# Kernel tuning notes

Measured on AMD Instinct MI355X. Metric: run time of the kernel, lower is better.

Reference implementation:

```python
import jax, jax.numpy as jnp
import numpy as np

N, D, H, E, K = 16384, 1024, 4096, 8, 2
EPS = 1e-5


def setup_inputs() -> dict:
    key = jax.random.key(0)
    ks = jax.random.split(key, 12)
    s = 0.02
    return {
        "x": jax.random.normal(ks[0], (N, D), dtype=jnp.float32),
        "ln_g": jnp.ones((D,), jnp.float32),
        "ln_b": jnp.zeros((D,), jnp.float32),
        "r_w1": jax.random.normal(ks[1], (D, H // 2), jnp.float32) * s,
        "r_b1": jnp.zeros((H // 2,), jnp.float32),
        "r_w2": jax.random.normal(ks[2], (H // 2, E), jnp.float32) * s,
        "r_b2": jnp.zeros((E,), jnp.float32),
        "e_w1": jax.random.normal(ks[3], (E, D, H), jnp.float32) * s,
        "e_b1": jnp.zeros((E, H), jnp.float32),
        "e_w2": jax.random.normal(ks[4], (E, H, D), jnp.float32) * s,
        "e_b2": jnp.zeros((E, D), jnp.float32),
    }


def reference(x, ln_g, ln_b, r_w1, r_b1, r_w2, r_b2, e_w1, e_b1, e_w2, e_b2):
    # LayerNorm
    mu = jnp.mean(x, axis=-1, keepdims=True)
    var = jnp.mean(jnp.square(x - mu), axis=-1, keepdims=True)
    xn = (x - mu) * jax.lax.rsqrt(var + EPS) * ln_g + ln_b  # [N, D]

    # Router: Linear -> ReLU -> Linear -> softmax -> top-k, renormalize
    logits = jax.nn.relu(xn @ r_w1 + r_b1) @ r_w2 + r_b2  # [N, E]
    probs = jax.nn.softmax(logits, axis=-1)
    vals, idx = jax.lax.top_k(probs, K)  # [N, K]
    vals = vals / jnp.sum(vals, axis=-1, keepdims=True)

    # Dense expert dispatch: loop over fixed small E, weight by combine gate
    out = jnp.zeros_like(x)
    for e in range(E):
        gate = jnp.sum(vals * (idx == e).astype(vals.dtype), axis=-1)  # [N]
        h = jax.nn.relu(xn @ e_w1[e] + e_b1[e])  # dropout in eval mode -> identity
        y = h @ e_w2[e] + e_b2[e]  # [N, D]
        out = out + gate[:, None] * y
    return x + out
```

## Files before the change

kernel.cpp:

```cpp
#include <hip/hip_runtime.h>
#include <cstdint>
#include <cstddef>

typedef unsigned short u16;
typedef __attribute__((ext_vector_type(8))) short bf16x8;
typedef __attribute__((ext_vector_type(4))) float f32x4;

#define N_TOK 16384
#define DIM   1024
#define HID   4096
#define NEXP  8
#define HR    2048
#define TAU   0.02f

__device__ __forceinline__ u16 f2bf(float f) {
  union { float f; uint32_t u; } x; x.f = f;
  uint32_t r = x.u + 0x7FFFu + ((x.u >> 16) & 1u);
  return (u16)(r >> 16);
}
__device__ __forceinline__ float bf2f(u16 u) {
  union { uint32_t u; float f; } x; x.u = ((uint32_t)u) << 16; return x.f;
}

__device__ __forceinline__ void async16(const void* g, const void* l) {
  auto gp = reinterpret_cast<const __attribute__((address_space(1))) uint32_t*>(
      reinterpret_cast<uintptr_t>(g));
  auto lp = reinterpret_cast<__attribute__((address_space(3))) uint32_t*>(
      reinterpret_cast<uintptr_t>(l));
  __builtin_amdgcn_global_load_lds(gp, lp, 16, 0, 0);
}

template<bool SPLIT>
__global__ __launch_bounds__(256)
void transpose_cvt(const float* __restrict__ src, u16* __restrict__ hi,
                   u16* __restrict__ lo, int R, int C)
{
  __shared__ float tile[32][33];
  const size_t bofs = (size_t)blockIdx.z * R * C;
  src += bofs; hi += bofs; if (SPLIT) lo += bofs;
  const int tx = threadIdx.x, ty = threadIdx.y;
  const int c0 = blockIdx.x * 32, r0 = blockIdx.y * 32;
#pragma unroll
  for (int i = 0; i < 4; ++i)
    tile[ty + i * 8][tx] = src[(size_t)(r0 + ty + i * 8) * C + c0 + tx];
  __syncthreads();
#pragma unroll
  for (int i = 0; i < 4; ++i) {
    float v = tile[tx][ty + i * 8];
    size_t o = (size_t)(c0 + ty + i * 8) * R + r0 + tx;
    u16 h = f2bf(v);
    hi[o] = h;
    if (SPLIT) lo[o] = f2bf(v - bf2f(h));
  }
}

__global__ __launch_bounds__(256)
void ln_kernel(const float* __restrict__ x, const float* __restrict__ g,
               const float* __restrict__ b, u16* __restrict__ xh,
               u16* __restrict__ xl, float* __restrict__ out)
{
  const int row = blockIdx.x;
  const int t = threadIdx.x;
  const float4 xv = ((const float4*)(x + (size_t)row * DIM))[t];
  float s = xv.x + xv.y + xv.z + xv.w;
  float q = xv.x * xv.x + xv.y * xv.y + xv.z * xv.z + xv.w * xv.w;
#pragma unroll
  for (int off = 32; off; off >>= 1) {
    s += __shfl_down(s, off, 64);
    q += __shfl_down(q, off, 64);
  }
  __shared__ float sm[8];
  __shared__ float mu_s, rs_s;
  const int lane = t & 63, wv = t >> 6;
  if (lane == 0) { sm[wv] = s; sm[wv + 4] = q; }
  __syncthreads();
  if (t == 0) {
    float S = sm[0] + sm[1] + sm[2] + sm[3];
    float Q = sm[4] + sm[5] + sm[6] + sm[7];
    float mu = S * (1.f / DIM);
    float var = Q * (1.f / DIM) - mu * mu;
    mu_s = mu; rs_s = rsqrtf(var + 1e-5f);
  }
  __syncthreads();
  const float mu = mu_s, rs = rs_s;
  const float4 gv = ((const float4*)g)[t];
  const float4 bv = ((const float4*)b)[t];
  float n0 = (xv.x - mu) * rs * gv.x + bv.x;
  float n1 = (xv.y - mu) * rs * gv.y + bv.y;
  float n2 = (xv.z - mu) * rs * gv.z + bv.z;
  float n3 = (xv.w - mu) * rs * gv.w + bv.w;
  ushort4 h, l;
  h.x = f2bf(n0); l.x = f2bf(n0 - bf2f(h.x));
  h.y = f2bf(n1); l.y = f2bf(n1 - bf2f(h.y));
  h.z = f2bf(n2); l.z = f2bf(n2 - bf2f(h.z));
  h.w = f2bf(n3); l.w = f2bf(n3 - bf2f(h.w));
  ((ushort4*)(xh + (size_t)row * DIM))[t] = h;
  ((ushort4*)(xl + (size_t)row * DIM))[t] = l;
  ((float4*)(out + (size_t)row * DIM))[t] = xv;
}

__global__ __launch_bounds__(256)
void logits_kernel(const u16* __restrict__ HrB, const float* __restrict__ w2,
                   float* __restrict__ logits)
{
  const int row = blockIdx.x, t = threadIdx.x;
  const u16* h = HrB + (size_t)row * HR;
  const ushort4* hv = (const ushort4*)(h + t * 8);
  ushort4 h0 = hv[0], h1 = hv[1];
  u16 hh[8] = {h0.x, h0.y, h0.z, h0.w, h1.x, h1.y, h1.z, h1.w};
  float p[8] = {0, 0, 0, 0, 0, 0, 0, 0};
#pragma unroll
  for (int j = 0; j < 8; ++j) {
    const int col = t * 8 + j;
    const float v = bf2f(hh[j]);
    const float4* wp = (const float4*)(w2 + (size_t)col * 8);
    float4 a = wp[0], b = wp[1];
    p[0] += v * a.x; p[1] += v * a.y; p[2] += v * a.z; p[3] += v * a.w;
    p[4] += v * b.x; p[5] += v * b.y; p[6] += v * b.z; p[7] += v * b.w;
  }
#pragma unroll
  for (int off = 32; off; off >>= 1)
#pragma unroll
    for (int e = 0; e < 8; ++e) p[e] += __shfl_down(p[e], off, 64);
  __shared__ float sm[4][8];
  const int lane = t & 63, wv = t >> 6;
  if (lane == 0) {
#pragma unroll
    for (int e = 0; e < 8; ++e) sm[wv][e] = p[e];
  }
  __syncthreads();
  if (t < 8)
    logits[(size_t)row * 8 + t] = sm[0][t] + sm[1][t] + sm[2][t] + sm[3][t];
}

__device__ __forceinline__ void load_logits(const float* logits, const float* b2,
                                            int row, float l[8]) {
  const float4* lp = (const float4*)(logits + (size_t)row * 8);
  float4 a = lp[0], b = lp[1];
  l[0] = a.x + b2[0]; l[1] = a.y + b2[1]; l[2] = a.z + b2[2]; l[3] = a.w + b2[3];
  l[4] = b.x + b2[4]; l[5] = b.y + b2[5]; l[6] = b.z + b2[6]; l[7] = b.w + b2[7];
}
__device__ __forceinline__ void top2(const float l[8], int& i0, float& l0,
                                     int& i1, float& l1) {
  i0 = 0; l0 = l[0];
#pragma unroll
  for (int e = 1; e < 8; ++e) if (l[e] > l0) { l0 = l[e]; i0 = e; }
  i1 = -1; l1 = -1e30f;
#pragma unroll
  for (int e = 0; e < 8; ++e) if (e != i0 && l[e] > l1) { l1 = l[e]; i1 = e; }
}

__global__ __launch_bounds__(256)
void pass_flag(float* __restrict__ logits, const float* __restrict__ b2,
               int* __restrict__ fixL, int* __restrict__ cntFix)
{
  __shared__ int lcnt;
  __shared__ int base;
  const int t = threadIdx.x;
  const int row = blockIdx.x * 256 + t;
  if (t == 0) lcnt = 0;
  float l[8]; load_logits(logits, b2, row, l);
  int i0, i1; float l0, l1;
  top2(l, i0, l0, i1, l1);
  float l2 = -1e30f;
#pragma unroll
  for (int e = 0; e < 8; ++e)
    if (e != i0 && e != i1 && l[e] > l2) l2 = l[e];
  const bool flag = (l1 - l2) < TAU;
  __syncthreads();
  int r = 0;
  if (flag) r = atomicAdd(&lcnt, 1);
  __syncthreads();
  if (t == 0) base = atomicAdd(cntFix, lcnt);
  __syncthreads();
  if (flag) {
    fixL[base + r] = row;
    float4 z = {0.f, 0.f, 0.f, 0.f};
    ((float4*)(logits + (size_t)row * 8))[0] = z;
    ((float4*)(logits + (size_t)row * 8))[1] = z;
  }
}

__global__ __launch_bounds__(256)
void pass_count(const float* __restrict__ logits, const float* __restrict__ b2,
                int* __restrict__ cnts)
{
  __shared__ int lcnt[NEXP];
  const int t = threadIdx.x;
  const int row = blockIdx.x * 256 + t;
  if (t < NEXP) lcnt[t] = 0;
  float l[8]; load_logits(logits, b2, row, l);
  int i0, i1; float l0, l1;
  top2(l, i0, l0, i1, l1);
  __syncthreads();
  atomicAdd(&lcnt[i0], 1);
  atomicAdd(&lcnt[i1], 1);
  __syncthreads();
  if (t < NEXP) atomicAdd(&cnts[t], lcnt[t]);
}

__global__ void scan_kernel(const int* __restrict__ cnts, int* __restrict__ offs)
{
  if (threadIdx.x == 0) {
    int s = 0;
#pragma unroll
    for (int e = 0; e < NEXP; ++e) { offs[e] = s; s += cnts[e]; }
    offs[NEXP] = s;
  }
}

__global__ __launch_bounds__(256)
void pass_scatter(const float* __restrict__ logits, const float* __restrict__ b2,
                  const int* __restrict__ offs, int* __restrict__ cnts2,
                  int* __restrict__ rowsC, float* __restrict__ gateC)
{
  __shared__ int lcnt[NEXP];
  __shared__ int sbase[NEXP];
  const int t = threadIdx.x;
  const int row = blockIdx.x * 256 + t;
  if (t < NEXP) lcnt[t] = 0;
  float l[8]; load_logits(logits, b2, row, l);
  int i0, i1; float l0, l1;
  top2(l, i0, l0, i1, l1);
  float tt = expf(l1 - l0);
  float g0 = 1.f / (1.f + tt);
  float g1 = tt / (1.f + tt);
  __syncthreads();
  int r0 = atomicAdd(&lcnt[i0], 1);
  int r1 = atomicAdd(&lcnt[i1], 1);
  __syncthreads();
  if (t < NEXP) sbase[t] = atomicAdd(&cnts2[t], lcnt[t]);
  __syncthreads();
  int p0 = offs[i0] + sbase[i0] + r0;
  int p1 = offs[i1] + sbase[i1] + r1;
  rowsC[p0] = row; gateC[p0] = g0;
  rowsC[p1] = row; gateC[p1] = g1;
}

template<bool SPLIT, int EPI, bool GATHER, bool FUSED>
__global__ __launch_bounds__(256, 2)
void gemm_bt(const u16* __restrict__ A0, const u16* __restrict__ A1,
             const u16* __restrict__ B0, const u16* __restrict__ B1,
             int lda, int ldb, int K, int M,
             size_t bStrideE, int biasStrideE,
             const int* __restrict__ counts, int expertArg,
             const int* __restrict__ offs,
             const int* __restrict__ rowsC, const float* __restrict__ gatesC,
             const float* __restrict__ bias,
             const float* __restrict__ w2, float* __restrict__ logits,
             u16* __restrict__ Cbf, float* __restrict__ Cf32, int ldc)
{
  const int expert = FUSED ? (int)blockIdx.z : expertArg;
  const int Mq = counts ? counts[expert] : M;
  const int m0 = blockIdx.y * 128;
  if (m0 >= Mq) return;
  const int n0 = blockIdx.x * 128;
  const int off = offs ? offs[expert] : 0;
  const int* rows = rowsC ? rowsC + off : nullptr;
  const float* gates = gatesC ? gatesC + off : nullptr;
  const u16* B = B0 + (FUSED ? (size_t)expert * bStrideE : 0);
  const u16* Bl = SPLIT ? B1 : nullptr;
  const float* bi = bias + (FUSED ? (size_t)expert * biasStrideE : 0);
  const int z = FUSED ? 0 : (int)blockIdx.z;
  const int zOff = z * K;

  __shared__ u16 As0[128 * 32], Bs0[128 * 32];
  __shared__ u16 As1[SPLIT ? 128 * 32 : 8], Bs1[SPLIT ? 128 * 32 : 8];

  const int t = threadIdx.x;
  size_t aoff[2]; int acodd[2]; size_t boff[2];
#pragma unroll
  for (int i = 0; i < 2; ++i) {
    int gdx = i * 256 + t;
    int ar = gdx >> 2, ac = (gdx & 3) * 8;
    int am = m0 + ar;
    int amc = am < Mq ? am : (Mq - 1);
    int agr = GATHER ? rows[amc] : amc;
    if (FUSED && EPI == 2) agr += off;
    aoff[i] = (size_t)agr * lda + ac + zOff;
    boff[i] = (size_t)(n0 + ar) * ldb + ac + zOff;
    acodd[i] = gdx * 8;
  }

  f32x4 acc[4][4];
#pragma unroll
  for (int i = 0; i < 4; ++i)
#pragma unroll
    for (int j = 0; j < 4; ++j) acc[i][j] = (f32x4){0.f, 0.f, 0.f, 0.f};

  const int lane = t & 63, wv = t >> 6;
  const int wm = (wv >> 1) * 64, wn = (wv & 1) * 64;
  const int fr = lane & 15, fq = lane >> 4;

  for (int k0 = 0; k0 < K; k0 += 32) {
    __syncthreads();
#pragma unroll
    for (int i = 0; i < 2; ++i) {
      async16(A0 + aoff[i] + k0, &As0[acodd[i]]);
      async16(B + boff[i] + k0, &Bs0[acodd[i]]);
      if (SPLIT) {
        async16(A1 + aoff[i] + k0, &As1[acodd[i]]);
        async16(Bl + boff[i] + k0, &Bs1[acodd[i]]);
      }
    }
    __syncthreads();
    bf16x8 af[4], bfr[4], af1[4], bf1[4];
#pragma unroll
    for (int xi = 0; xi < 4; ++xi) {
      af[xi]  = *(const bf16x8*)&As0[(wm + xi * 16 + fr) * 32 + fq * 8];
      bfr[xi] = *(const bf16x8*)&Bs0[(wn + xi * 16 + fr) * 32 + fq * 8];
      if (SPLIT) {
        af1[xi] = *(const bf16x8*)&As1[(wm + xi * 16 + fr) * 32 + fq * 8];
        bf1[xi] = *(const bf16x8*)&Bs1[(wn + xi * 16 + fr) * 32 + fq * 8];
      }
    }
#pragma unroll
    for (int mt = 0; mt < 4; ++mt)
#pragma unroll
      for (int nt = 0; nt < 4; ++nt) {
        acc[mt][nt] = __builtin_amdgcn_mfma_f32_16x16x32_bf16(af[mt], bfr[nt], acc[mt][nt], 0, 0, 0);
        if (SPLIT) {
          acc[mt][nt] = __builtin_amdgcn_mfma_f32_16x16x32_bf16(af[mt], bf1[nt], acc[mt][nt], 0, 0, 0);
          acc[mt][nt] = __builtin_amdgcn_mfma_f32_16x16x32_bf16(af1[mt], bfr[nt], acc[mt][nt], 0, 0, 0);
        }
      }
  }

  if constexpr (EPI == 3) {
    float w2v[4][8]; float b1v[4];
#pragma unroll
    for (int nt = 0; nt < 4; ++nt) {
      const int n = n0 + wn + nt * 16 + fr;
      b1v[nt] = bi[n];
      const float4* wp = (const float4*)(w2 + (size_t)n * 8);
      float4 wa = wp[0], wb = wp[1];
      w2v[nt][0] = wa.x; w2v[nt][1] = wa.y; w2v[nt][2] = wa.z; w2v[nt][3] = wa.w;
      w2v[nt][4] = wb.x; w2v[nt][5] = wb.y; w2v[nt][6] = wb.z; w2v[nt][7] = wb.w;
    }
#pragma unroll
    for (int mt = 0; mt < 4; ++mt) {
      float pe[4][8];
#pragma unroll
      for (int r = 0; r < 4; ++r)
#pragma unroll
        for (int e = 0; e < 8; ++e) pe[r][e] = 0.f;
#pragma unroll
      for (int nt = 0; nt < 4; ++nt)
#pragma unroll
        for (int r = 0; r < 4; ++r) {
          float v = fmaxf(acc[mt][nt][r] + b1v[nt], 0.f);
#pragma unroll
          for (int e = 0; e < 8; ++e) pe[r][e] += v * w2v[nt][e];
        }
#pragma unroll
      for (int offx = 1; offx < 16; offx <<= 1)
#pragma unroll
        for (int r = 0; r < 4; ++r)
#pragma unroll
          for (int e = 0; e < 8; ++e)
            pe[r][e] += __shfl_xor(pe[r][e], offx, 64);
      if (fr == 0) {
#pragma unroll
        for (int r = 0; r < 4; ++r) {
          const int m = m0 + wm + mt * 16 + fq * 4 + r;
          if (m < Mq) {
            const int lrow = GATHER ? rows[m] : m;
#pragma unroll
            for (int e = 0; e < 8; ++e)
              atomicAdd(&logits[(size_t)lrow * 8 + e], pe[r][e]);
          }
        }
      }
    }
    return;
  }

#pragma unroll
  for (int mt = 0; mt < 4; ++mt) {
#pragma unroll
    for (int nt = 0; nt < 4; ++nt) {
      const int n = n0 + wn + nt * 16 + fr;
      const float bv = (z == 0) ? bi[n] : 0.f;
#pragma unroll
      for (int r = 0; r < 4; ++r) {
        const int m = m0 + wm + mt * 16 + fq * 4 + r;
        if (m < Mq) {
          float v = acc[mt][nt][r] + bv;
          if constexpr (EPI == 1) {
            const int crow = m + (FUSED ? off : 0);
            Cbf[(size_t)crow * ldc + n] = f2bf(fmaxf(v, 0.f));
          } else {
            atomicAdd(&Cf32[(size_t)rows[m] * ldc + n], gates[m] * v);
          }
        }
      }
    }
  }
}

extern "C" void kernel_launch(void* const* d_in, const int* in_sizes, int n_in,
                              void* d_out, int out_size, void* d_ws, size_t ws_size,
                              hipStream_t stream)
{
  const float* x    = (const float*)d_in[0];
  const float* ln_g = (const float*)d_in[1];
  const float* ln_b = (const float*)d_in[2];
  const float* r_w1 = (const float*)d_in[3];
  const float* r_b1 = (const float*)d_in[4];
  const float* r_w2 = (const float*)d_in[5];
  const float* r_b2 = (const float*)d_in[6];
  const float* e_w1 = (const float*)d_in[7];
  const float* e_b1 = (const float*)d_in[8];
  const float* e_w2 = (const float*)d_in[9];
  const float* e_b2 = (const float*)d_in[10];
  float* out = (float*)d_out;

  char* ws = (char*)d_ws;
  const size_t MB = 1024ull * 1024ull;
  u16*   xnhi = (u16*)(ws);
  u16*   xnlo = (u16*)(ws + 32 * MB);
  u16*   rw1h = (u16*)(ws + 64 * MB);
  u16*   rw1l = (u16*)(ws + 68 * MB);
  u16*   ew1t = (u16*)(ws + 72 * MB);
  u16*   ew2t = (u16*)(ws + 136 * MB);
  float* logits = (float*)(ws + 200 * MB);
  int*   rowsC  = (int*)(ws + 200 * MB + 512 * 1024);
  float* gateC  = (float*)(ws + 200 * MB + 640 * 1024);
  int*   fixL   = (int*)(ws + 200 * MB + 768 * 1024);
  int*   cntb   = (int*)(ws + 200 * MB + 832 * 1024);
  int*   cnts   = cntb;
  int*   cnts2  = cntb + 8;
  int*   offs   = cntb + 16;
  int*   cntFix = cntb + 25;
  u16*   Hbuf = (u16*)(ws + 201 * MB);
  u16*   HrB  = Hbuf;
  (void)in_sizes; (void)n_in; (void)out_size;

  const bool fused = ws_size >= 458ull * MB;

  hipMemsetAsync(cntb, 0, 256, stream);

  dim3 tb(32, 8);
  transpose_cvt<true ><<<dim3(HR / 32, DIM / 32, 1), tb, 0, stream>>>(r_w1, rw1h, rw1l, DIM, HR);
  transpose_cvt<false><<<dim3(HID / 32, DIM / 32, NEXP), tb, 0, stream>>>(e_w1, ew1t, nullptr, DIM, HID);
  transpose_cvt<false><<<dim3(DIM / 32, HID / 32, NEXP), tb, 0, stream>>>(e_w2, ew2t, nullptr, HID, DIM);

  ln_kernel<<<N_TOK, 256, 0, stream>>>(x, ln_g, ln_b, xnhi, xnlo, out);

  gemm_bt<false, 1, false, false><<<dim3(HR / 128, N_TOK / 128), 256, 0, stream>>>(
      xnhi, nullptr, rw1h, nullptr, DIM, DIM, DIM, N_TOK, 0, 0,
      nullptr, 0, nullptr, nullptr, nullptr, r_b1, nullptr, nullptr,
      HrB, nullptr, HR);

  logits_kernel<<<N_TOK, 256, 0, stream>>>(HrB, r_w2, logits);

  pass_flag<<<N_TOK / 256, 256, 0, stream>>>(logits, r_b2, fixL, cntFix);

  gemm_bt<true, 3, true, false><<<dim3(HR / 128, N_TOK / 128), 256, 0, stream>>>(
      xnhi, xnlo, rw1h, rw1l, DIM, DIM, DIM, N_TOK, 0, 0,
      cntFix, 0, nullptr, fixL, nullptr, r_b1, r_w2, logits,
      nullptr, nullptr, 0);

  pass_count<<<N_TOK / 256, 256, 0, stream>>>(logits, r_b2, cnts);
  scan_kernel<<<1, 64, 0, stream>>>(cnts, offs);
  pass_scatter<<<N_TOK / 256, 256, 0, stream>>>(logits, r_b2, offs, cnts2, rowsC, gateC);

  if (fused) {
    gemm_bt<false, 1, true, true><<<dim3(HID / 128, N_TOK / 128, NEXP), 256, 0, stream>>>(
        xnhi, nullptr, ew1t, nullptr, DIM, DIM, DIM, N_TOK,
        (size_t)HID * DIM, HID,
        cnts, 0, offs, rowsC, nullptr, e_b1, nullptr, nullptr,
        Hbuf, nullptr, HID);
    gemm_bt<false, 2, false, true><<<dim3(DIM / 128, N_TOK / 128, NEXP), 256, 0, stream>>>(
        Hbuf, nullptr, ew2t, nullptr, HID, HID, HID, N_TOK,
        (size_t)DIM * HID, DIM,
        cnts, 0, offs, rowsC, gateC, e_b2, nullptr, nullptr,
        nullptr, out, DIM);
  } else {
    for (int e = 0; e < NEXP; ++e) {
      gemm_bt<false, 1, true, false><<<dim3(HID / 128, N_TOK / 128), 256, 0, stream>>>(
          xnhi, nullptr, ew1t + (size_t)e * HID * DIM, nullptr,
          DIM, DIM, DIM, N_TOK, 0, 0,
          cnts, e, offs, rowsC, nullptr, e_b1 + (size_t)e * HID, nullptr, nullptr,
          Hbuf, nullptr, HID);
      gemm_bt<false, 2, false, false><<<dim3(DIM / 128, N_TOK / 128, 2), 256, 0, stream>>>(
          Hbuf, nullptr, ew2t + (size_t)e * DIM * HID, nullptr,
          HID, HID, HID / 2, N_TOK, 0, 0,
          cnts, e, offs, rowsC, gateC, e_b2 + (size_t)e * DIM, nullptr, nullptr,
          nullptr, out, DIM);
    }
  }
}
```

Before: 1.605 ms.

## Compact MoE expert GEMM grids by tile offsets and swizzle blocks across XCDs

The fused expert GEMMs now launch a 1D grid sized for at most 264 row tiles instead of a full 3D grid of 8 experts times all row tiles. Each block maps to an (expert, row tile, column tile) through prefix tile offsets computed in the scan kernel, so far fewer blocks exit immediately. An XCD-aware swizzle is also applied to the fused and dense router GEMMs so that neighbouring tiles land on the same XCD and share L2 more. This adds an expert lookup per block and depends on the MAXMT bound covering every possible routing.

```diff
diff --git a/kernel.cpp b/kernel.cpp
--- a/kernel.cpp
+++ b/kernel.cpp
@@ -12,6 +12,7 @@
 #define NEXP  8
 #define HR    2048
 #define TAU   0.02f
+#define MAXMT 264
 
 __device__ __forceinline__ u16 f2bf(float f) {
   union { float f; uint32_t u; } x; x.f = f;
@@ -28,6 +29,12 @@
   auto lp = reinterpret_cast<__attribute__((address_space(3))) uint32_t*>(
       reinterpret_cast<uintptr_t>(l));
   __builtin_amdgcn_global_load_lds(gp, lp, 16, 0, 0);
+}
+
+__device__ __forceinline__ unsigned xcd_swz(unsigned flat, unsigned nwg) {
+  const unsigned xcd = flat & 7u, lid = flat >> 3;
+  const unsigned q = nwg >> 3, r = nwg & 7u;
+  return (xcd < r ? xcd * (q + 1u) : r * (q + 1u) + (xcd - r) * q) + lid;
 }
 
 template<bool SPLIT>
@@ -199,13 +206,18 @@
   if (t < NEXP) atomicAdd(&cnts[t], lcnt[t]);
 }
 
-__global__ void scan_kernel(const int* __restrict__ cnts, int* __restrict__ offs)
+__global__ void scan_kernel(const int* __restrict__ cnts, int* __restrict__ offs,
+                            int* __restrict__ tileOffs)
 {
   if (threadIdx.x == 0) {
-    int s = 0;
-#pragma unroll
-    for (int e = 0; e < NEXP; ++e) { offs[e] = s; s += cnts[e]; }
+    int s = 0, ts = 0;
+#pragma unroll
+    for (int e = 0; e < NEXP; ++e) {
+      offs[e] = s; s += cnts[e];
+      tileOffs[e] = ts; ts += (cnts[e] + 127) >> 7;
+    }
     offs[NEXP] = s;
+    tileOffs[NEXP] = ts;
   }
 }
 
@@ -244,17 +256,39 @@
              int lda, int ldb, int K, int M,
              size_t bStrideE, int biasStrideE,
              const int* __restrict__ counts, int expertArg,
-             const int* __restrict__ offs,
+             const int* __restrict__ offs, const int* __restrict__ tileOffs,
              const int* __restrict__ rowsC, const float* __restrict__ gatesC,
              const float* __restrict__ bias,
              const float* __restrict__ w2, float* __restrict__ logits,
              u16* __restrict__ Cbf, float* __restrict__ Cf32, int ldc)
 {
-  const int expert = FUSED ? (int)blockIdx.z : expertArg;
+  int expert, m0, n0;
+  if constexpr (FUSED) {
+    const int NT = expertArg;
+    const unsigned swz = xcd_swz(blockIdx.x, gridDim.x);
+    const int mt = (int)(swz / (unsigned)NT);
+    if (mt >= tileOffs[NEXP]) return;
+    int e = 0;
+#pragma unroll
+    for (int i = 1; i < NEXP; ++i) if (tileOffs[i] <= mt) e = i;
+    expert = e;
+    m0 = (mt - tileOffs[e]) * 128;
+    n0 = (int)(swz % (unsigned)NT) * 128;
+  } else if (counts == nullptr) {
+    const unsigned nwg = gridDim.x * gridDim.y;
+    const unsigned flat = blockIdx.y * gridDim.x + blockIdx.x;
+    const unsigned swz = xcd_swz(flat, nwg);
+    expert = expertArg;
+    m0 = (int)(swz / gridDim.x) * 128;
+    n0 = (int)(swz % gridDim.x) * 128;
+  } else {
+    expert = expertArg;
+    m0 = blockIdx.y * 128;
+    n0 = blockIdx.x * 128;
+  }
+
   const int Mq = counts ? counts[expert] : M;
-  const int m0 = blockIdx.y * 128;
   if (m0 >= Mq) return;
-  const int n0 = blockIdx.x * 128;
   const int off = offs ? offs[expert] : 0;
   const int* rows = rowsC ? rowsC + off : nullptr;
   const float* gates = gatesC ? gatesC + off : nullptr;
@@ -432,6 +466,7 @@
   int*   cnts2  = cntb + 8;
   int*   offs   = cntb + 16;
   int*   cntFix = cntb + 25;
+  int*   tileOffs = cntb + 32;
   u16*   Hbuf = (u16*)(ws + 201 * MB);
   u16*   HrB  = Hbuf;
   (void)in_sizes; (void)n_in; (void)out_size;
@@ -449,7 +484,7 @@
 
   gemm_bt<false, 1, false, false><<<dim3(HR / 128, N_TOK / 128), 256, 0, stream>>>(
       xnhi, nullptr, rw1h, nullptr, DIM, DIM, DIM, N_TOK, 0, 0,
-      nullptr, 0, nullptr, nullptr, nullptr, r_b1, nullptr, nullptr,
+      nullptr, 0, nullptr, nullptr, nullptr, nullptr, r_b1, nullptr, nullptr,
       HrB, nullptr, HR);
 
   logits_kernel<<<N_TOK, 256, 0, stream>>>(HrB, r_w2, logits);
@@ -458,35 +493,35 @@
 
   gemm_bt<true, 3, true, false><<<dim3(HR / 128, N_TOK / 128), 256, 0, stream>>>(
       xnhi, xnlo, rw1h, rw1l, DIM, DIM, DIM, N_TOK, 0, 0,
-      cntFix, 0, nullptr, fixL, nullptr, r_b1, r_w2, logits,
+      cntFix, 0, nullptr, nullptr, fixL, nullptr, r_b1, r_w2, logits,
       nullptr, nullptr, 0);
 
   pass_count<<<N_TOK / 256, 256, 0, stream>>>(logits, r_b2, cnts);
-  scan_kernel<<<1, 64, 0, stream>>>(cnts, offs);
+  scan_kernel<<<1, 64, 0, stream>>>(cnts, offs, tileOffs);
   pass_scatter<<<N_TOK / 256, 256, 0, stream>>>(logits, r_b2, offs, cnts2, rowsC, gateC);
 
   if (fused) {
-    gemm_bt<false, 1, true, true><<<dim3(HID / 128, N_TOK / 128, NEXP), 256, 0, stream>>>(
+    gemm_bt<false, 1, true, true><<<dim3((HID / 128) * MAXMT), 256, 0, stream>>>(
         xnhi, nullptr, ew1t, nullptr, DIM, DIM, DIM, N_TOK,
         (size_t)HID * DIM, HID,
-        cnts, 0, offs, rowsC, nullptr, e_b1, nullptr, nullptr,
+        cnts, HID / 128, offs, tileOffs, rowsC, nullptr, e_b1, nullptr, nullptr,
         Hbuf, nullptr, HID);
-    gemm_bt<false, 2, false, true><<<dim3(DIM / 128, N_TOK / 128, NEXP), 256, 0, stream>>>(
+    gemm_bt<false, 2, false, true><<<dim3((DIM / 128) * MAXMT), 256, 0, stream>>>(
         Hbuf, nullptr, ew2t, nullptr, HID, HID, HID, N_TOK,
         (size_t)DIM * HID, DIM,
-        cnts, 0, offs, rowsC, gateC, e_b2, nullptr, nullptr,
+        cnts, DIM / 128, offs, tileOffs, rowsC, gateC, e_b2, nullptr, nullptr,
         nullptr, out, DIM);
   } else {
     for (int e = 0; e < NEXP; ++e) {
       gemm_bt<false, 1, true, false><<<dim3(HID / 128, N_TOK / 128), 256, 0, stream>>>(
           xnhi, nullptr, ew1t + (size_t)e * HID * DIM, nullptr,
           DIM, DIM, DIM, N_TOK, 0, 0,
-          cnts, e, offs, rowsC, nullptr, e_b1 + (size_t)e * HID, nullptr, nullptr,
+          cnts, e, offs, nullptr, rowsC, nullptr, e_b1 + (size_t)e * HID, nullptr, nullptr,
           Hbuf, nullptr, HID);
       gemm_bt<false, 2, false, false><<<dim3(DIM / 128, N_TOK / 128, 2), 256, 0, stream>>>(
           Hbuf, nullptr, ew2t + (size_t)e * DIM * HID, nullptr,
           HID, HID, HID / 2, N_TOK, 0, 0,
-          cnts, e, offs, rowsC, gateC, e_b2 + (size_t)e * DIM, nullptr, nullptr,
+          cnts, e, offs, nullptr, rowsC, gateC, e_b2 + (size_t)e * DIM, nullptr, nullptr,
           nullptr, out, DIM);
     }
   }
```

Measured after the change: 1.578 ms. Within noise of the previous version (-1.7%).
